# Kernel optimization log

Hardware: AMD Instinct MI355X
Metric: run time of the kernel (lower is better)

Reference implementation:

```python
import jax, jax.numpy as jnp
import numpy as np

F = 32          # final_feature_size
S = 256         # coordinate stride for key packing (coords < 251, offsets +-1)
SENT = 2 ** 30  # sentinel key > any real packed key
DELTAS = [dx * S * S + dy * S + dz
          for dx in (-1, 0, 1) for dy in (-1, 0, 1) for dz in (-1, 0, 1)]  # 27 kernel offsets


def setup_inputs() -> dict:
    rng = np.random.default_rng(0)
    T, per_frame, B, Npts = 16, 40000, 2, 400000
    # --- history sweep voxels: coords [t, x, y, z], t = global frame id ---
    t = np.repeat(np.arange(T, dtype=np.int32), per_frame)
    xyz = rng.integers(1, 251, size=(T * per_frame, 3), dtype=np.int32)
    keys = ((t.astype(np.int64) * S + xyz[:, 0]) * S + xyz[:, 1]) * S + xyz[:, 2]
    _, idx = np.unique(keys, return_index=True)  # ME quantization dedup
    t, xyz = t[idx], xyz[idx]
    n = t.shape[0]
    history_coordinates = np.concatenate([t[:, None], xyz], axis=1).astype(np.int32)
    history_batches = (t // (T // B)).astype(np.int32)  # scene id per voxel
    history_features = rng.standard_normal((n, 1)).astype(np.float32)
    # --- current scan query points ---
    b = rng.integers(0, B, size=Npts).astype(np.int32)
    qxyz = rng.integers(1, 251, size=(Npts, 3), dtype=np.int32)
    curr_coords = np.concatenate([b[:, None], qxyz], axis=1).astype(np.int32)
    points = np.concatenate([b[:, None].astype(np.float32),
                             qxyz.astype(np.float32),
                             rng.standard_normal((Npts, 1)).astype(np.float32)], axis=1)
    # --- params ---
    W_bb = (rng.standard_normal((27, 1, F)) * (2.0 / 27) ** 0.5).astype(np.float32)
    W_conv = (rng.standard_normal((27, F, F)) * (1.0 / (27 * F)) ** 0.5).astype(np.float32)
    return {
        'history_features': jnp.asarray(history_features),
        'points': jnp.asarray(points),
        'W_bb': jnp.asarray(W_bb),
        'W_conv': jnp.asarray(W_conv),
        'history_coordinates': jnp.asarray(history_coordinates),
        'history_batches': jnp.asarray(history_batches),
        'curr_coords': jnp.asarray(curr_coords),
    }


def pack4(c):
    c = c.astype(jnp.int32)
    return ((c[:, 0] * S + c[:, 1]) * S + c[:, 2]) * S + c[:, 3]


def sparse_conv(sorted_keys, table_feats, out_keys, W):
    """Minkowski-style sparse conv: gather neighbor at each of 27 offsets, matmul, scatter-add."""
    n = sorted_keys.shape[0]
    out = jnp.zeros((out_keys.shape[0], W.shape[2]), table_feats.dtype)
    for i, d in enumerate(DELTAS):
        nk = out_keys + d
        pos = jnp.clip(jnp.searchsorted(sorted_keys, nk), 0, n - 1)
        valid = (sorted_keys[pos] == nk)[:, None]
        g = jnp.where(valid, table_feats[pos], 0.0)
        out = out + g @ W[i]
    return out


def reference(history_features, points, W_bb, W_conv,
              history_coordinates, history_batches, curr_coords):
    n = history_features.shape[0]
    # ---- history backbone (stand-in: one sparse 3x3x3 conv, 1->F, time col as batch) ----
    keys_h = pack4(history_coordinates)
    order = jnp.argsort(keys_h)
    bb = sparse_conv(keys_h[order], history_features[order], keys_h, W_bb)  # [n, F]
    # ---- MinkowskiMaxPooling kernel [1000,1,1,1]: max over time per (b,x,y,z) ----
    pool_coords = jnp.concatenate([history_batches[:, None], history_coordinates[:, 1:4]], axis=1)
    keys_p = pack4(pool_coords)
    uk, inv = jnp.unique(keys_p, return_inverse=True, size=n, fill_value=SENT)  # sorted
    pooled = jax.ops.segment_max(bb, inv, num_segments=n)                        # [n, F]
    # ---- current_conv evaluated at (unique) query voxels, then slice back to points ----
    keys_q = pack4(curr_coords)
    m = keys_q.shape[0]
    uq, qinv = jnp.unique(keys_q, return_inverse=True, size=m, fill_value=SENT)
    conv_q = sparse_conv(uk, pooled, uq, W_conv)  # [m, F]
    ofield = conv_q[qinv]                          # TensorField slice: per-point features
    # ---- mode='update_point_features', preserve_feature==3 ----
    return jnp.concatenate([points[:, :4], ofield], axis=1)  # [Npts, 4+F]
```

## Files before the change

kernel.cpp:

```cpp
#include <hip/hip_runtime.h>
#include <stdint.h>
#include <utility>


#define TPB 256
#define SCAN_WPT 8
#define GB_H 2048
#define GB_P 256
#define NBLK_SCAN (GB_H + GB_P)
typedef unsigned long long u64;
typedef unsigned int u32;
typedef unsigned short u16;

#define FLAG_AGG (1ull << 62)
#define FLAG_PRE (2ull << 62)
#define FLAG_MSK (3ull << 62)

__device__ __forceinline__ u32 trans16(float x) {
    u32 b = __float_as_uint(x);
    u32 bf = (b + 0x7FFFu + ((b >> 16) & 1u)) >> 16;
    return ((bf & 0x8000u) ? (~bf) : (bf | 0x8000u)) & 0xFFFFu;
}
__device__ __forceinline__ float detrans16(u32 u) {
    u32 orig = (u & 0x8000u) ? (u & 0x7FFFu) : ((~u) & 0xFFFFu);
    return __uint_as_float(orig << 16);
}

template <int... Ks>
__device__ __forceinline__ void kfma(float pv, const float* __restrict__ W,
                                     float& acc,
                                     std::integer_sequence<int, Ks...>) {
    ((acc = fmaf(__uint_as_float((u32)__builtin_amdgcn_ds_swizzle(
                     (int)__float_as_uint(pv), (Ks << 5))),
                 W[Ks * 32], acc)),
     ...);
}

__global__ void build_bitmaps_kernel(const int4* __restrict__ hc,
                                     const int* __restrict__ hb,
                                     int n,
                                     u64* __restrict__ hist_bm,
                                     u64* __restrict__ pool_bm,
                                     u64* __restrict__ multi_bm,
                                     int2* __restrict__ kp) {
    int j = blockIdx.x * blockDim.x + threadIdx.x;
    if (j >= n) return;
    int4 c = hc[j];
    int key = ((c.x * 256 + c.y) * 256 + c.z) * 256 + c.w;
    atomicOr(&hist_bm[key >> 6], 1ull << (key & 63));
    int pk = ((hb[j] * 256 + c.y) * 256 + c.z) * 256 + c.w;
    kp[j] = make_int2(key, pk);
    u64 bit = 1ull << (pk & 63);
    u64 old = atomicOr(&pool_bm[pk >> 6], bit);
    if (old & bit) atomicOr(&multi_bm[pk >> 6], bit);
}

__global__ void scan_fused_kernel(const u64* __restrict__ hist_bm,
                                  const u64* __restrict__ pool_bm,
                                  u32* __restrict__ hist_rank,
                                  u32* __restrict__ pool_rank,
                                  const u64* __restrict__ multi_bm,
                                  u32* __restrict__ pooled,
                                  u64* __restrict__ st) {
    __shared__ u32 s[TPB];
    __shared__ u32 sbase;
    int t = threadIdx.x;
    bool isPool = blockIdx.x >= GB_H;
    const u64* bm = isPool ? pool_bm : hist_bm;
    u32* rank = isPool ? pool_rank : hist_rank;
    int blk = isPool ? (blockIdx.x - GB_H) : blockIdx.x;
    size_t base = ((size_t)blk * TPB + t) * SCAN_WPT;
    u32 pc[SCAN_WPT]; u32 acc = 0;
#pragma unroll
    for (int i = 0; i < SCAN_WPT; i++) { pc[i] = __popcll(bm[base + i]); acc += pc[i]; }
    s[t] = acc; __syncthreads();
    for (int off = 1; off < TPB; off <<= 1) {
        u32 x = (t >= off) ? s[t - off] : 0;
        __syncthreads();
        s[t] += x;
        __syncthreads();
    }
    u32 wave_excl = s[t] - acc;
    u32 blocksum = s[TPB - 1];

    int segStart = isPool ? GB_H : 0;
    if (t < 64) {
        if (blockIdx.x == segStart) {
            if (t == 0) {
                atomicExch(&st[blockIdx.x], FLAG_PRE | (u64)blocksum);
                sbase = 0;
            }
        } else {
            if (t == 0) atomicExch(&st[blockIdx.x], FLAG_AGG | (u64)blocksum);
            u64 run = 0;
            int end = blockIdx.x;
            while (true) {
                int i = end - 1 - t;
                u64 v = (i >= segStart) ? atomicAdd(&st[i], 0ull)
                                        : FLAG_AGG;
                u64 fl = v & FLAG_MSK;
                u64 pre_mask   = __ballot(fl == FLAG_PRE);
                u64 unpub_mask = __ballot(fl == 0ull);
                int first_pre   = pre_mask   ? (__ffsll((long long)pre_mask) - 1)   : 64;
                int first_unpub = unpub_mask ? (__ffsll((long long)unpub_mask) - 1) : 64;
                if (first_pre < first_unpub) {
                    u32 contrib = (t <= first_pre) ? (u32)(v & 0xFFFFFFFFull) : 0u;
#pragma unroll
                    for (int off = 1; off < 64; off <<= 1)
                        contrib += (u32)__shfl_xor((int)contrib, off);
                    run += contrib;
                    break;
                } else if (first_unpub == 64) {
                    u32 contrib = (u32)(v & 0xFFFFFFFFull);
#pragma unroll
                    for (int off = 1; off < 64; off <<= 1)
                        contrib += (u32)__shfl_xor((int)contrib, off);
                    run += contrib;
                    end -= 64;
                }
            }
            if (t == 0) {
                atomicExch(&st[blockIdx.x], FLAG_PRE | (run + (u64)blocksum));
                sbase = (u32)run;
            }
        }
    }
    __syncthreads();

    u32 run = sbase + wave_excl;
    u32 run0 = run;
#pragma unroll
    for (int i = 0; i < SCAN_WPT; i++) { rank[base + i] = run; run += pc[i]; }
    if (isPool) {
        u32 r2 = run0;
#pragma unroll
        for (int i = 0; i < SCAN_WPT; i++) {
            u64 mw = multi_bm[base + i];
            if (mw) {
                u64 pw = bm[base + i];
                while (mw) {
                    int b = __ffsll((long long)mw) - 1;
                    mw &= mw - 1;
                    u32 slot = r2 + (u32)__popcll(pw & ((1ull << b) - 1ull));
                    u32* row = pooled + (size_t)slot * 16;
#pragma unroll
                    for (int w2 = 0; w2 < 16; w2++) row[w2] = 0u;
                }
            }
            r2 += pc[i];
        }
    }
}

__global__ __launch_bounds__(TPB, 8)
void bb_pool_kernel(const int2* __restrict__ kp,
                    const float* __restrict__ hf,
                    const float* __restrict__ Wbb,
                    int n,
                    const u64* __restrict__ hist_bm,
                    const u32* __restrict__ hist_rank,
                    const u64* __restrict__ pool_bm,
                    const u32* __restrict__ pool_rank,
                    const u64* __restrict__ multi_bm,
                    u32* __restrict__ pooled) {
    int nwg = gridDim.x;
    int q = nwg >> 3, r = nwg & 7;
    int xcd = blockIdx.x & 7, idx = blockIdx.x >> 3;
    int swz = (xcd < r ? xcd * (q + 1) : r * (q + 1) + (xcd - r) * q) + idx;

    int p = (swz * TPB + threadIdx.x) >> 5;
    if (p >= n) return;
    int lane = threadIdx.x & 63;
    int hb32 = lane & 32;
    int f = lane & 31;

    int2 k2 = kp[p];
    int key = k2.x, pk = k2.y;
    __builtin_assume(key >= 65793 && key < (1 << 28));
    __builtin_assume(pk >= 65793 && pk < (1 << 25));

    u64 pword = pool_bm[pk >> 6];
    u32 prank = pool_rank[pk >> 6];
    u64 mword = multi_bm[pk >> 6];

    float fv = 0.f;
    bool hit = false;
    if (f < 27) {
        int t1 = f / 9, rem = f - t1 * 9, t2 = rem / 3, t3 = rem - t2 * 3;
        int nk = key + (t1 - 1) * 65536 + (t2 - 1) * 256 + (t3 - 1);
        __builtin_assume(nk >= 0 && nk < (1 << 28));
        u64 word = hist_bm[nk >> 6];
        u32 rk   = hist_rank[nk >> 6];
        if ((word >> (nk & 63)) & 1ull) {
            u32 r2 = rk + (u32)__popcll(word & ((1ull << (nk & 63)) - 1ull));
            __builtin_assume(r2 < (1u << 20));
            fv = hf[r2];
            hit = true;
        }
    }
    unsigned long long bal = __ballot(hit);
    u32 mymask = (u32)(bal >> hb32);

    float acc = 0.f;
    while (mymask) {
        int b = __ffs(mymask) - 1;
        mymask &= mymask - 1;
        float fb = __shfl(fv, hb32 + b);
        acc = fmaf(fb, Wbb[b * 32 + f], acc);
    }

    int bit = pk & 63;
    int slot = (int)(prank + (u32)__popcll(pword & ((1ull << bit) - 1ull)));
    __builtin_assume(slot >= 0);
    bool multi = (mword >> bit) & 1ull;

    u32 tv = trans16(acc);
    u32 packed = tv | (((u32)__shfl_down((int)tv, 1)) << 16);
    if ((f & 1) == 0) {
        u32* addr = pooled + (size_t)slot * 16 + (f >> 1);
        if (!multi) {
            *addr = packed;
        } else {
            u32 oldv = *addr;
            while (true) {
                u32 lo = max(oldv & 0xFFFFu, packed & 0xFFFFu);
                u32 hi = max(oldv >> 16, packed >> 16);
                u32 mx = lo | (hi << 16);
                if (mx == oldv) break;
                u32 prev = atomicCAS(addr, oldv, mx);
                if (prev == oldv) break;
                oldv = prev;
            }
        }
    }
}

__global__ __launch_bounds__(TPB, 8)
void query_kernel(const int4* __restrict__ qc,
                  const float* __restrict__ pts,
                  const float* __restrict__ Wc,
                  int m,
                  const u64* __restrict__ pool_bm,
                  const u32* __restrict__ pool_rank,
                  const u16* __restrict__ pooled16,
                  float* __restrict__ out) {
    int p = (blockIdx.x * blockDim.x + threadIdx.x) >> 5;
    if (p >= m) return;
    int lane = threadIdx.x & 63;
    int hb32 = lane & 32;
    int f = lane & 31;

    int4 c = qc[p];
    int qk = ((c.x * 256 + c.y) * 256 + c.z) * 256 + c.w;
    __builtin_assume(qk >= 65793 && qk < (1 << 25));

    int slotL = -1;
    if (f < 27) {
        int t1 = f / 9, rem = f - t1 * 9, t2 = rem / 3, t3 = rem - t2 * 3;
        int nk = qk + (t1 - 1) * 65536 + (t2 - 1) * 256 + (t3 - 1);
        __builtin_assume(nk >= 0 && nk < (1 << 25));
        u64 word = pool_bm[nk >> 6];
        u32 rk   = pool_rank[nk >> 6];
        if ((word >> (nk & 63)) & 1ull)
            slotL = (int)(rk + (u32)__popcll(word & ((1ull << (nk & 63)) - 1ull)));
    }
    unsigned long long bal = __ballot(slotL >= 0);
    u32 mymask = (u32)(bal >> hb32);

    float acc = 0.f;
    while (mymask) {
        int b = __ffs(mymask) - 1;
        mymask &= mymask - 1;
        int slot = __shfl(slotL, hb32 + b);
        __builtin_assume(slot >= 0 && slot < (1 << 20));
        float pv = detrans16(pooled16[(size_t)slot * 32 + f]);
        const float* W = Wc + b * 1024 + f;
        kfma(pv, W, acc, std::make_integer_sequence<int, 32>{});
    }

    float acc2 = __shfl_down(acc, 1);
    if ((f & 1) == 0) {
        float2 st; st.x = acc; st.y = acc2;
        *(float2*)(out + (size_t)p * 36 + 4 + f) = st;
    }
    if (f < 4) out[(size_t)p * 36 + f] = pts[p * 5 + f];
}

extern "C" void kernel_launch(void* const* d_in, const int* in_sizes, int n_in,
                              void* d_out, int out_size, void* d_ws, size_t ws_size,
                              hipStream_t stream) {
    const float* hfeat   = (const float*)d_in[0];
    const float* pts     = (const float*)d_in[1];
    const float* Wbb     = (const float*)d_in[2];
    const float* Wconv   = (const float*)d_in[3];
    const int4*  hcoords = (const int4*)d_in[4];
    const int*   hbatch  = (const int*)d_in[5];
    const int4*  qcoords = (const int4*)d_in[6];
    int n = in_sizes[0];
    int m = in_sizes[1] / 5;

    const int NW_H = 1 << 22;
    const int NW_P = 1 << 19;

    char* w = (char*)d_ws;
    char* zbase = w;
    u64* hist_bm      = (u64*)w;       w += (size_t)NW_H * 8;
    u64* pool_bm      = (u64*)w;       w += (size_t)NW_P * 8;
    u64* multi_bm     = (u64*)w;       w += (size_t)NW_P * 8;
    u64* st           = (u64*)w;       w += (size_t)NBLK_SCAN * 8;
    size_t zbytes = (size_t)(w - zbase);
    u32* pooled       = (u32*)w;       w += (size_t)n * 64;
    u32* hist_rank    = (u32*)w;       w += (size_t)NW_H * 4;
    u32* pool_rank    = (u32*)w;       w += (size_t)NW_P * 4;
    int2* kp          = (int2*)w;      w += (size_t)n * 8;

    (void)hipMemsetAsync(zbase, 0x00, zbytes, stream);

    int gb_n   = (n + TPB - 1) / TPB;
    int gb_n32 = (int)(((long long)n * 32 + TPB - 1) / TPB);
    int gb_m32 = (int)(((long long)m * 32 + TPB - 1) / TPB);

    build_bitmaps_kernel<<<gb_n, TPB, 0, stream>>>(hcoords, hbatch, n,
                                                   hist_bm, pool_bm, multi_bm, kp);
    scan_fused_kernel<<<NBLK_SCAN, TPB, 0, stream>>>(hist_bm, pool_bm,
                                                     hist_rank, pool_rank,
                                                     multi_bm, pooled, st);
    bb_pool_kernel<<<gb_n32, TPB, 0, stream>>>(kp, hfeat, Wbb, n,
                                               hist_bm, hist_rank,
                                               pool_bm, pool_rank, multi_bm, pooled);
    query_kernel<<<gb_m32, TPB, 0, stream>>>(qcoords, pts, Wconv, m,
                                             pool_bm, pool_rank,
                                             (const u16*)pooled, (float*)d_out);
}
```

Before: 255.2 us.

## Interleave bitmap words with rank prefix into 16-byte rank-select entries

Replaces the separate bitmap-word and rank arrays used for neighbor lookups with packed 16-byte entries, each holding 96 bitmap bits and their prefix rank. Each lookup then needs one aligned 16-byte load instead of two scattered loads, cutting memory transactions in the gather-heavy backbone and query kernels. The scan kernel is reorganized to handle three words per thread, needs a larger grid and writes the packed entries. In exchange, lookups need a divide-by-three index computation and extra branching for bits in the upper 32-bit part of an entry.

```diff
diff --git a/kernel.cpp b/kernel.cpp
--- a/kernel.cpp
+++ b/kernel.cpp
@@ -4,10 +4,9 @@
 
 
 #define TPB 256
-#define SCAN_WPT 8
-#define GB_H 2048
-#define GB_P 256
-#define NBLK_SCAN (GB_H + GB_P)
+#define GB_H2 5462
+#define GB_P2 683
+#define NBLK_SCAN (GB_H2 + GB_P2)
 typedef unsigned long long u64;
 typedef unsigned int u32;
 typedef unsigned short u16;
@@ -15,6 +14,10 @@
 #define FLAG_AGG (1ull << 62)
 #define FLAG_PRE (2ull << 62)
 #define FLAG_MSK (3ull << 62)
+
+__device__ __forceinline__ u32 div3(u32 x) {
+    return (u32)(((u64)x * 0xAAAAAAABull) >> 33);
+}
 
 __device__ __forceinline__ u32 trans16(float x) {
     u32 b = __float_as_uint(x);
@@ -57,33 +60,36 @@
 
 __global__ void scan_fused_kernel(const u64* __restrict__ hist_bm,
                                   const u64* __restrict__ pool_bm,
-                                  u32* __restrict__ hist_rank,
-                                  u32* __restrict__ pool_rank,
+                                  uint4* __restrict__ hist_ent,
+                                  uint4* __restrict__ pool_ent,
                                   const u64* __restrict__ multi_bm,
                                   u32* __restrict__ pooled,
                                   u64* __restrict__ st) {
     __shared__ u32 s[TPB];
     __shared__ u32 sbase;
     int t = threadIdx.x;
-    bool isPool = blockIdx.x >= GB_H;
+    bool isPool = blockIdx.x >= GB_H2;
     const u64* bm = isPool ? pool_bm : hist_bm;
-    u32* rank = isPool ? pool_rank : hist_rank;
-    int blk = isPool ? (blockIdx.x - GB_H) : blockIdx.x;
-    size_t base = ((size_t)blk * TPB + t) * SCAN_WPT;
-    u32 pc[SCAN_WPT]; u32 acc = 0;
-#pragma unroll
-    for (int i = 0; i < SCAN_WPT; i++) { pc[i] = __popcll(bm[base + i]); acc += pc[i]; }
-    s[t] = acc; __syncthreads();
+    uint4* ent = isPool ? pool_ent : hist_ent;
+    int NW = isPool ? (1 << 19) : (1 << 22);
+    int blk = isPool ? (blockIdx.x - GB_H2) : blockIdx.x;
+    size_t w0i = ((size_t)blk * TPB + t) * 3;
+    u64 w0 = (w0i     < (size_t)NW) ? bm[w0i]     : 0ull;
+    u64 w1 = (w0i + 1 < (size_t)NW) ? bm[w0i + 1] : 0ull;
+    u64 w2 = (w0i + 2 < (size_t)NW) ? bm[w0i + 2] : 0ull;
+    u32 pc0 = (u32)__popcll(w0), pc1 = (u32)__popcll(w1), pc2 = (u32)__popcll(w2);
+    u32 pcT = pc0 + pc1 + pc2;
+    s[t] = pcT; __syncthreads();
     for (int off = 1; off < TPB; off <<= 1) {
         u32 x = (t >= off) ? s[t - off] : 0;
         __syncthreads();
         s[t] += x;
         __syncthreads();
     }
-    u32 wave_excl = s[t] - acc;
+    u32 wave_excl = s[t] - pcT;
     u32 blocksum = s[TPB - 1];
 
-    int segStart = isPool ? GB_H : 0;
+    int segStart = isPool ? GB_H2 : 0;
     if (t < 64) {
         if (blockIdx.x == segStart) {
             if (t == 0) {
@@ -128,26 +134,33 @@
     __syncthreads();
 
     u32 run = sbase + wave_excl;
-    u32 run0 = run;
+    u32 lo1 = (u32)w1;
+    u32 e0 = ((u32)blk * TPB + (u32)t) * 2;
+    ent[e0] = make_uint4((u32)w0, (u32)(w0 >> 32), lo1, run);
+    u64 a1 = (w1 >> 32) | (w2 << 32);
+    u32 r1 = run + pc0 + (u32)__popc(lo1);
+    ent[e0 + 1] = make_uint4((u32)a1, (u32)(a1 >> 32), (u32)(w2 >> 32), r1);
+
+    if (isPool) {
+        u32 rw0 = run, rw1 = run + pc0, rw2 = run + pc0 + pc1;
+        u64 wv[3] = {w0, w1, w2};
+        u32 rv[3] = {rw0, rw1, rw2};
 #pragma unroll
-    for (int i = 0; i < SCAN_WPT; i++) { rank[base + i] = run; run += pc[i]; }
-    if (isPool) {
-        u32 r2 = run0;
+        for (int i = 0; i < 3; i++) {
+            if (w0i + i < (size_t)NW) {
+                u64 mw = multi_bm[w0i + i];
+                if (mw) {
+                    u64 pw = wv[i];
+                    while (mw) {
+                        int b = __ffsll((long long)mw) - 1;
+                        mw &= mw - 1;
+                        u32 slot = rv[i] + (u32)__popcll(pw & ((1ull << b) - 1ull));
+                        u32* row = pooled + (size_t)slot * 16;
 #pragma unroll
-        for (int i = 0; i < SCAN_WPT; i++) {
-            u64 mw = multi_bm[base + i];
-            if (mw) {
-                u64 pw = bm[base + i];
-                while (mw) {
-                    int b = __ffsll((long long)mw) - 1;
-                    mw &= mw - 1;
-                    u32 slot = r2 + (u32)__popcll(pw & ((1ull << b) - 1ull));
-                    u32* row = pooled + (size_t)slot * 16;
-#pragma unroll
-                    for (int w2 = 0; w2 < 16; w2++) row[w2] = 0u;
+                        for (int q2 = 0; q2 < 16; q2++) row[q2] = 0u;
+                    }
                 }
             }
-            r2 += pc[i];
         }
     }
 }
@@ -157,10 +170,8 @@
                     const float* __restrict__ hf,
                     const float* __restrict__ Wbb,
                     int n,
-                    const u64* __restrict__ hist_bm,
-                    const u32* __restrict__ hist_rank,
-                    const u64* __restrict__ pool_bm,
-                    const u32* __restrict__ pool_rank,
+                    const uint4* __restrict__ hist_ent,
+                    const uint4* __restrict__ pool_ent,
                     const u64* __restrict__ multi_bm,
                     u32* __restrict__ pooled) {
     int nwg = gridDim.x;
@@ -179,8 +190,9 @@
     __builtin_assume(key >= 65793 && key < (1 << 28));
     __builtin_assume(pk >= 65793 && pk < (1 << 25));
 
-    u64 pword = pool_bm[pk >> 6];
-    u32 prank = pool_rank[pk >> 6];
+    u32 ep = div3((u32)pk >> 5);
+    u32 offp = (u32)pk - ep * 96u;
+    uint4 PE = pool_ent[ep];
     u64 mword = multi_bm[pk >> 6];
 
     float fv = 0.f;
@@ -189,10 +201,18 @@
         int t1 = f / 9, rem = f - t1 * 9, t2 = rem / 3, t3 = rem - t2 * 3;
         int nk = key + (t1 - 1) * 65536 + (t2 - 1) * 256 + (t3 - 1);
         __builtin_assume(nk >= 0 && nk < (1 << 28));
-        u64 word = hist_bm[nk >> 6];
-        u32 rk   = hist_rank[nk >> 6];
-        if ((word >> (nk & 63)) & 1ull) {
-            u32 r2 = rk + (u32)__popcll(word & ((1ull << (nk & 63)) - 1ull));
+        u32 e = div3((u32)nk >> 5);
+        u32 off = (u32)nk - e * 96u;
+        uint4 E = hist_ent[e];
+        u64 a = ((u64)E.y << 32) | E.x;
+        bool lo = off < 64u;
+        u32 offh = (off - 64u) & 31u;
+        u32 bitv = lo ? (u32)((a >> (off & 63u)) & 1ull)
+                      : ((E.z >> offh) & 1u);
+        if (bitv) {
+            u32 sub = lo ? (u32)__popcll(a & ((1ull << (off & 63u)) - 1ull))
+                         : (u32)__popcll(a) + (u32)__popc(E.z & ((1u << offh) - 1u));
+            u32 r2 = E.w + sub;
             __builtin_assume(r2 < (1u << 20));
             fv = hf[r2];
             hit = true;
@@ -209,10 +229,14 @@
         acc = fmaf(fb, Wbb[b * 32 + f], acc);
     }
 
-    int bit = pk & 63;
-    int slot = (int)(prank + (u32)__popcll(pword & ((1ull << bit) - 1ull)));
+    u64 pa = ((u64)PE.y << 32) | PE.x;
+    bool plo = offp < 64u;
+    u32 offph = (offp - 64u) & 31u;
+    u32 psub = plo ? (u32)__popcll(pa & ((1ull << (offp & 63u)) - 1ull))
+                   : (u32)__popcll(pa) + (u32)__popc(PE.z & ((1u << offph) - 1u));
+    int slot = (int)(PE.w + psub);
     __builtin_assume(slot >= 0);
-    bool multi = (mword >> bit) & 1ull;
+    bool multi = (mword >> (pk & 63)) & 1ull;
 
     u32 tv = trans16(acc);
     u32 packed = tv | (((u32)__shfl_down((int)tv, 1)) << 16);
@@ -223,9 +247,9 @@
         } else {
             u32 oldv = *addr;
             while (true) {
-                u32 lo = max(oldv & 0xFFFFu, packed & 0xFFFFu);
-                u32 hi = max(oldv >> 16, packed >> 16);
-                u32 mx = lo | (hi << 16);
+                u32 lo2 = max(oldv & 0xFFFFu, packed & 0xFFFFu);
+                u32 hi2 = max(oldv >> 16, packed >> 16);
+                u32 mx = lo2 | (hi2 << 16);
                 if (mx == oldv) break;
                 u32 prev = atomicCAS(addr, oldv, mx);
                 if (prev == oldv) break;
@@ -240,8 +264,7 @@
                   const float* __restrict__ pts,
                   const float* __restrict__ Wc,
                   int m,
-                  const u64* __restrict__ pool_bm,
-                  const u32* __restrict__ pool_rank,
+                  const uint4* __restrict__ pool_ent,
                   const u16* __restrict__ pooled16,
                   float* __restrict__ out) {
     int p = (blockIdx.x * blockDim.x + threadIdx.x) >> 5;
@@ -259,10 +282,19 @@
         int t1 = f / 9, rem = f - t1 * 9, t2 = rem / 3, t3 = rem - t2 * 3;
         int nk = qk + (t1 - 1) * 65536 + (t2 - 1) * 256 + (t3 - 1);
         __builtin_assume(nk >= 0 && nk < (1 << 25));
-        u64 word = pool_bm[nk >> 6];
-        u32 rk   = pool_rank[nk >> 6];
-        if ((word >> (nk & 63)) & 1ull)
-            slotL = (int)(rk + (u32)__popcll(word & ((1ull << (nk & 63)) - 1ull)));
+        u32 e = div3((u32)nk >> 5);
+        u32 off = (u32)nk - e * 96u;
+        uint4 E = pool_ent[e];
+        u64 a = ((u64)E.y << 32) | E.x;
+        bool lo = off < 64u;
+        u32 offh = (off - 64u) & 31u;
+        u32 bitv = lo ? (u32)((a >> (off & 63u)) & 1ull)
+                      : ((E.z >> offh) & 1u);
+        if (bitv) {
+            u32 sub = lo ? (u32)__popcll(a & ((1ull << (off & 63u)) - 1ull))
+                         : (u32)__popcll(a) + (u32)__popc(E.z & ((1u << offh) - 1u));
+            slotL = (int)(E.w + sub);
+        }
     }
     unsigned long long bal = __ballot(slotL >= 0);
     u32 mymask = (u32)(bal >> hb32);
@@ -301,6 +333,8 @@
 
     const int NW_H = 1 << 22;
     const int NW_P = 1 << 19;
+    const size_t EH_ALLOC = (size_t)GB_H2 * TPB * 2;
+    const size_t EP_ALLOC = (size_t)GB_P2 * TPB * 2;
 
     char* w = (char*)d_ws;
     char* zbase = w;
@@ -310,8 +344,8 @@
     u64* st           = (u64*)w;       w += (size_t)NBLK_SCAN * 8;
     size_t zbytes = (size_t)(w - zbase);
     u32* pooled       = (u32*)w;       w += (size_t)n * 64;
-    u32* hist_rank    = (u32*)w;       w += (size_t)NW_H * 4;
-    u32* pool_rank    = (u32*)w;       w += (size_t)NW_P * 4;
+    uint4* hist_ent   = (uint4*)w;     w += EH_ALLOC * 16;
+    uint4* pool_ent   = (uint4*)w;     w += EP_ALLOC * 16;
     int2* kp          = (int2*)w;      w += (size_t)n * 8;
 
     (void)hipMemsetAsync(zbase, 0x00, zbytes, stream);
@@ -323,12 +357,12 @@
     build_bitmaps_kernel<<<gb_n, TPB, 0, stream>>>(hcoords, hbatch, n,
                                                    hist_bm, pool_bm, multi_bm, kp);
     scan_fused_kernel<<<NBLK_SCAN, TPB, 0, stream>>>(hist_bm, pool_bm,
-                                                     hist_rank, pool_rank,
+                                                     hist_ent, pool_ent,
                                                      multi_bm, pooled, st);
     bb_pool_kernel<<<gb_n32, TPB, 0, stream>>>(kp, hfeat, Wbb, n,
-                                               hist_bm, hist_rank,
-                                               pool_bm, pool_rank, multi_bm, pooled);
+                                               hist_ent, pool_ent,
+                                               multi_bm, pooled);
     query_kernel<<<gb_m32, TPB, 0, stream>>>(qcoords, pts, Wconv, m,
-                                             pool_bm, pool_rank,
+                                             pool_ent,
                                              (const u16*)pooled, (float*)d_out);
 }
```

After: 272.9 us. +6.9%, slower.
